# Kernel optimization log

Hardware: AMD Instinct MI355X
Metric: run time of the kernel (lower is better)

## Reference

```python
import jax, jax.numpy as jnp
import numpy as np

B, S, D, H = 32, 512, 256, 512  # batch, seq_len, input_dim, hidden_dim (512 hardcoded in source)


def setup_inputs() -> dict:
    key = jax.random.key(0)
    ks = jax.random.split(key, 24)
    sc = 1.0 / np.sqrt(H)

    def p(k, shape):
        return (jax.random.normal(k, shape, jnp.float32) * sc).astype(jnp.float32)

    return {
        "x": jax.random.normal(ks[0], (B, S, D), jnp.float32),
        # encoder forward direction (PyTorch LSTM gate order i,f,g,o)
        "Wih_f": p(ks[1], (4 * H, D)), "Whh_f": p(ks[2], (4 * H, H)), "b_f": p(ks[3], (4 * H,)),
        # encoder reverse direction
        "Wih_r": p(ks[4], (4 * H, D)), "Whh_r": p(ks[5], (4 * H, H)), "b_r": p(ks[6], (4 * H,)),
        # decoder LSTM (input never used: decoder_input is always zeros in the source)
        "Wih_d": p(ks[7], (4 * H, H)), "Whh_d": p(ks[8], (4 * H, H)), "b_d": p(ks[9], (4 * H,)),
        # reduce_h / reduce_c
        "Wr_h": p(ks[10], (H, 2 * H)), "br_h": p(ks[11], (H,)),
        "Wr_c": p(ks[12], (H, 2 * H)), "br_c": p(ks[13], (H,)),
        # pointer attention
        "W1": p(ks[14], (H, H)), "b1": p(ks[15], (H,)),
        "W2": p(ks[16], (H, H)), "b2": p(ks[17], (H,)),
        "vt": p(ks[18], (1, H)), "bvt": p(ks[19], (1,)),
    }


def _lstm_cell(h, c, z):
    i, f, g, o = jnp.split(z, 4, axis=-1)
    c_new = jax.nn.sigmoid(f) * c + jax.nn.sigmoid(i) * jnp.tanh(g)
    h_new = jax.nn.sigmoid(o) * jnp.tanh(c_new)
    return h_new, c_new


def _run_lstm(xs, Wih, Whh, b):
    """xs: [S, B, D] -> (outputs [S,B,H], h_T [B,H], c_T [B,H])"""
    Bn = xs.shape[1]
    Hn = Whh.shape[1]
    init = (jnp.zeros((Bn, Hn), xs.dtype), jnp.zeros((Bn, Hn), xs.dtype))
    x_proj = jnp.einsum('sbd,gd->sbg', xs, Wih) + b  # precompute input contribution

    def step(carry, xp):
        h, c = carry
        h, c = _lstm_cell(h, c, xp + h @ Whh.T)
        return (h, c), h

    (hT, cT), hs = jax.lax.scan(step, init, x_proj)
    return hs, hT, cT


def reference(x, Wih_f, Whh_f, b_f, Wih_r, Whh_r, b_r,
              Wih_d, Whh_d, b_d, Wr_h, br_h, Wr_c, br_c,
              W1, b1, W2, b2, vt, bvt):
    xs = jnp.swapaxes(x, 0, 1)  # [S, B, D]
    hs_f, hf, cf = _run_lstm(xs, Wih_f, Whh_f, b_f)
    hs_r, hr, cr = _run_lstm(xs[::-1], Wih_r, Whh_r, b_r)
    hs_r = hs_r[::-1]

    h_d = jnp.concatenate([hf, hr], axis=-1) @ Wr_h.T + br_h  # [B, H]
    c_d = jnp.concatenate([cf, cr], axis=-1) @ Wr_c.T + br_c

    enc_red = hs_f + hs_r  # [S, B, H]  (enc_out[...,:512] + enc_out[...,512:])
    pre1 = jnp.einsum('sbh,kh->sbk', enc_red, W1) + b1  # W1(enc) precomputed once

    seq_len = x.shape[1]

    def dec_step(carry, _):
        h, c = carry
        # decoder_input is always zeros -> Wih_d contribution is exactly 0
        h, c = _lstm_cell(h, c, h @ Whh_d.T + b_d)
        att = jnp.tanh(pre1 + (h @ W2.T + b2)[None])      # [S, B, H]
        scores = jnp.einsum('sbh,h->sb', att, vt[0]) + bvt[0]
        return (h, c), scores.T  # [B, S]

    _, logits = jax.lax.scan(dec_step, (h_d, c_d), None, length=seq_len)
    return jnp.swapaxes(logits, 0, 1)  # [B, seq_len, S]
```

## Files before the change

### kernel.cpp

```cpp
#include <hip/hip_runtime.h>
#include <hip/hip_bf16.h>
#include <cstdint>
#include <cstddef>

#define B_ 32
#define S_ 512
#define D_ 256
#define H_ 512

typedef _Float16 h2 __attribute__((ext_vector_type(2)));
typedef _Float16 h4 __attribute__((ext_vector_type(4)));
typedef _Float16 h8 __attribute__((ext_vector_type(8)));
typedef float f32x4 __attribute__((ext_vector_type(4)));
typedef unsigned u32x4 __attribute__((ext_vector_type(4)));

__device__ __forceinline__ h2 H2(unsigned u) { return __builtin_bit_cast(h2, u); }
__device__ __forceinline__ unsigned U2(h2 v) { return __builtin_bit_cast(unsigned, v); }

#if __has_builtin(__builtin_amdgcn_fdot2)
__device__ __forceinline__ float dot2f(h2 a, h2 b, float c) {
  return __builtin_amdgcn_fdot2(a, b, c, false);
}
#else
__device__ __forceinline__ float dot2f(h2 a, h2 b, float c) {
  return c + (float)a.x * (float)b.x + (float)a.y * (float)b.y;
}
#endif

#if __has_builtin(__builtin_amdgcn_exp2f)
__device__ __forceinline__ float exp2_fast(float x) { return __builtin_amdgcn_exp2f(x); }
#else
__device__ __forceinline__ float exp2_fast(float x) { return exp2f(x); }
#endif
#if __has_builtin(__builtin_amdgcn_rcpf)
__device__ __forceinline__ float rcp_fast(float x) { return __builtin_amdgcn_rcpf(x); }
#else
__device__ __forceinline__ float rcp_fast(float x) { return 1.0f / x; }
#endif

__device__ __forceinline__ float sigm(float x) {
  return rcp_fast(1.0f + exp2_fast(-1.4426950408889634f * x));
}
__device__ __forceinline__ float tanh_fast(float x) {
  return 1.0f - 2.0f * rcp_fast(1.0f + exp2_fast(2.8853900817779268f * x));
}

__device__ __forceinline__ uint4 coh_load16(const void* p) {
  u32x4 v;
  asm volatile("global_load_dwordx4 %0, %1, off sc0 sc1"
               : "=v"(v) : "v"(p) : "memory");
  return __builtin_bit_cast(uint4, v);
}
__device__ __forceinline__ void vm_drain() {
  asm volatile("s_waitcnt vmcnt(0)" ::: "memory");
}

__device__ __forceinline__ bool valid16(uint4 v) {
  return ((v.x & 0xFFFFu) != 0xFFFFu) && ((v.x >> 16) != 0xFFFFu) &&
         ((v.y & 0xFFFFu) != 0xFFFFu) && ((v.y >> 16) != 0xFFFFu) &&
         ((v.z & 0xFFFFu) != 0xFFFFu) && ((v.z >> 16) != 0xFFFFu) &&
         ((v.w & 0xFFFFu) != 0xFFFFu) && ((v.w >> 16) != 0xFFFFu);
}

__device__ __forceinline__ void h_store(unsigned short* p, unsigned short v) {
  __hip_atomic_store(p, v, __ATOMIC_RELAXED, __HIP_MEMORY_SCOPE_AGENT);
}

__global__ __launch_bounds__(256) void fill_sent_k(uint4* __restrict__ dst, size_t n16) {
  uint4 s = {0xFFFFFFFFu, 0xFFFFFFFFu, 0xFFFFFFFFu, 0xFFFFFFFFu};
  size_t stride = (size_t)gridDim.x * 256;
  for (size_t i = (size_t)blockIdx.x * 256 + threadIdx.x; i < n16; i += stride)
    dst[i] = s;
}

__global__ __launch_bounds__(256) void f2h_k(const float* __restrict__ src,
                                             _Float16* __restrict__ dst, int n4) {
  int i = blockIdx.x * 256 + threadIdx.x;
  if (i < n4) {
    float4 v = ((const float4*)src)[i];
    h4 o = {(_Float16)v.x, (_Float16)v.y, (_Float16)v.z, (_Float16)v.w};
    ((h4*)dst)[i] = o;
  }
}

__global__ __launch_bounds__(256, 1) void enc_coop_k(
    const _Float16* __restrict__ xh,
    const _Float16* __restrict__ WihF, const _Float16* __restrict__ WhhF, const float* __restrict__ bF,
    const _Float16* __restrict__ WihR, const _Float16* __restrict__ WhhR, const float* __restrict__ bR,
    float* __restrict__ cF, float* __restrict__ cR,
    _Float16* __restrict__ hsF, _Float16* __restrict__ hsR)
{
  __shared__ __align__(16) _Float16 cbuf[96][16][8];
  __shared__ float zfin[4][16][17];
  __shared__ float cls[16][17];

  const int bid = blockIdx.x;
  const int group = bid >> 5;
  const int dir = group >> 1;
  const int bh0 = (group & 1) << 4;
  const int jb = bid & 31;
  const int c0 = jb << 4;
  const int tid = threadIdx.x;
  const int lane = tid & 63;
  const int wv = tid >> 6;

  const _Float16* __restrict__ Wih = dir ? WihR : WihF;
  const _Float16* __restrict__ Whh = dir ? WhhR : WhhF;
  const float* __restrict__ bias = dir ? bR : bF;
  _Float16* __restrict__ hs = dir ? hsR : hsF;
  float* __restrict__ cOut = dir ? cR : cF;

  h8 aw[24];
  {
    const int m = lane & 15, kg = lane >> 4;
    const int wrow = wv * H_ + c0 + m;
    const _Float16* wi = Wih + (size_t)wrow * D_;
    const _Float16* wh = Whh + (size_t)wrow * H_;
    #pragma unroll
    for (int tu = 0; tu < 24; ++tu) {
      int k = tu * 32 + kg * 8;
      aw[tu] = (k < 256) ? *(const h8*)(wi + k) : *(const h8*)(wh + (k - 256));
    }
  }

  const int cc = tid & 15, cb = tid >> 4;
  float bvg[4];
  #pragma unroll
  for (int g = 0; g < 4; ++g) bvg[g] = bias[g * H_ + c0 + cc];

  const char* cbase = (const char*)cbuf + (size_t)((lane >> 4) * 256 + (lane & 15) * 16);
  const int sn = tid & 15;
  const int xo = (tid >> 4) * 2;
  const int ho = (tid >> 4) * 4;
  __syncthreads();

  for (int t = 0; t < S_; ++t) {
    const int xi = dir ? (S_ - 1 - t) : t;

    {
      const _Float16* xp = xh + ((size_t)(bh0 + sn) * S_ + xi) * D_;
      uint4 v0 = *(const uint4*)(xp + xo * 8);
      uint4 v1 = *(const uint4*)(xp + xo * 8 + 8);
      *(uint4*)&cbuf[xo][sn][0] = v0;
      *(uint4*)&cbuf[xo + 1][sn][0] = v1;
    }
    __syncthreads();

    f32x4 acc = {0.f, 0.f, 0.f, 0.f};
    #pragma unroll
    for (int tu = 0; tu < 8; ++tu) {
      h8 bf = *(const h8*)(cbase + tu * 1024);
      acc = __builtin_amdgcn_mfma_f32_16x16x32_f16(aw[tu], bf, acc, 0, 0, 0);
    }

    {
      if (t == 0) {
        uint4 z = {0, 0, 0, 0};
        #pragma unroll
        for (int u = 0; u < 4; ++u) *(uint4*)&cbuf[32 + ho + u][sn][0] = z;
      } else {
        const int xip = dir ? xi + 1 : xi - 1;
        const _Float16* hbase = hs + ((size_t)xip * B_ + bh0 + sn) * H_;
        uint4 vs[4];
        unsigned pend = 0xF;
        do {
          #pragma unroll
          for (int u = 0; u < 4; ++u)
            if (pend & (1u << u)) vs[u] = coh_load16(hbase + (ho + u) * 8);
          vm_drain();
          #pragma unroll
          for (int u = 0; u < 4; ++u)
            if ((pend & (1u << u)) && valid16(vs[u])) pend &= ~(1u << u);
        } while (pend);
        #pragma unroll
        for (int u = 0; u < 4; ++u) *(uint4*)&cbuf[32 + ho + u][sn][0] = vs[u];
      }
    }
    __syncthreads();

    #pragma unroll
    for (int tu = 8; tu < 24; ++tu) {
      h8 bf = *(const h8*)(cbase + tu * 1024);
      acc = __builtin_amdgcn_mfma_f32_16x16x32_f16(aw[tu], bf, acc, 0, 0, 0);
    }
    {
      const int mrow = (lane >> 4) * 4, n = lane & 15;
      #pragma unroll
      for (int r = 0; r < 4; ++r) zfin[wv][mrow + r][n] = acc[r];
    }
    __syncthreads();

    {
      const float zi = zfin[0][cc][cb] + bvg[0];
      const float zf = zfin[1][cc][cb] + bvg[1];
      const float zg = zfin[2][cc][cb] + bvg[2];
      const float zo = zfin[3][cc][cb] + bvg[3];
      const float c_old = (t == 0) ? 0.f : cls[cc][cb];
      const float cn = sigm(zf) * c_old + sigm(zi) * tanh_fast(zg);
      const float hn = sigm(zo) * tanh_fast(cn);
      cls[cc][cb] = cn;
      _Float16 hh = (_Float16)hn;
      h_store((unsigned short*)(hs + ((size_t)xi * B_ + bh0 + cb) * H_ + c0 + cc),
              __builtin_bit_cast(unsigned short, hh));
      if (t == S_ - 1) cOut[(size_t)(bh0 + cb) * H_ + c0 + cc] = cn;
    }
    __syncthreads();
  }
}

__global__ __launch_bounds__(256, 1) void dec_coop_k(
    const float* __restrict__ hd0, const float* __restrict__ cD0,
    const _Float16* __restrict__ Whh, const float* __restrict__ bias,
    _Float16* __restrict__ hdec)
{
  __shared__ __align__(16) _Float16 cbuf[64][16][8];
  __shared__ float zfin[4][16][17];
  __shared__ float cls[16][17];

  const int bid = blockIdx.x;
  const int group = bid >> 5;
  const int bh0 = group << 4;
  const int jb = bid & 31;
  const int c0 = jb << 4;
  const int tid = threadIdx.x;
  const int lane = tid & 63;
  const int wv = tid >> 6;

  h8 aw[16];
  {
    const int m = lane & 15, kg = lane >> 4;
    const _Float16* wh = Whh + (size_t)(wv * H_ + c0 + m) * H_;
    #pragma unroll
    for (int tu = 0; tu < 16; ++tu) aw[tu] = *(const h8*)(wh + tu * 32 + kg * 8);
  }

  const int cc = tid & 15, cb = tid >> 4;
  float bvg[4];
  #pragma unroll
  for (int g = 0; g < 4; ++g) bvg[g] = bias[g * H_ + c0 + cc];
  cls[cc][cb] = cD0[(size_t)(bh0 + cb) * H_ + c0 + cc];

  const char* cbase = (const char*)cbuf + (size_t)((lane >> 4) * 256 + (lane & 15) * 16);
  const int sn = tid & 15, ho = (tid >> 4) * 4;
  __syncthreads();

  for (int t = 0; t < S_; ++t) {
    {
      if (t == 0) {
        const float* src = hd0 + (size_t)(bh0 + sn) * H_;
        #pragma unroll
        for (int u = 0; u < 4; ++u) {
          float4 f0 = *(const float4*)(src + (ho + u) * 8);
          float4 f1 = *(const float4*)(src + (ho + u) * 8 + 4);
          h8 o = {(_Float16)f0.x, (_Float16)f0.y, (_Float16)f0.z, (_Float16)f0.w,
                  (_Float16)f1.x, (_Float16)f1.y, (_Float16)f1.z, (_Float16)f1.w};
          *(h8*)&cbuf[ho + u][sn][0] = o;
        }
      } else {
        const _Float16* src = hdec + ((size_t)(t - 1) * B_ + bh0 + sn) * H_;
        uint4 vs[4];
        unsigned pend = 0xF;
        do {
          #pragma unroll
          for (int u = 0; u < 4; ++u)
            if (pend & (1u << u)) vs[u] = coh_load16(src + (ho + u) * 8);
          vm_drain();
          #pragma unroll
          for (int u = 0; u < 4; ++u)
            if ((pend & (1u << u)) && valid16(vs[u])) pend &= ~(1u << u);
        } while (pend);
        #pragma unroll
        for (int u = 0; u < 4; ++u) *(uint4*)&cbuf[ho + u][sn][0] = vs[u];
      }
    }
    __syncthreads();

    f32x4 acc = {0.f, 0.f, 0.f, 0.f};
    #pragma unroll
    for (int tu = 0; tu < 16; ++tu) {
      h8 bf = *(const h8*)(cbase + tu * 1024);
      acc = __builtin_amdgcn_mfma_f32_16x16x32_f16(aw[tu], bf, acc, 0, 0, 0);
    }
    {
      const int mrow = (lane >> 4) * 4, n = lane & 15;
      #pragma unroll
      for (int r = 0; r < 4; ++r) zfin[wv][mrow + r][n] = acc[r];
    }
    __syncthreads();

    {
      const float zi = zfin[0][cc][cb] + bvg[0];
      const float zf = zfin[1][cc][cb] + bvg[1];
      const float zg = zfin[2][cc][cb] + bvg[2];
      const float zo = zfin[3][cc][cb] + bvg[3];
      const float cn = sigm(zf) * cls[cc][cb] + sigm(zi) * tanh_fast(zg);
      const float hn = sigm(zo) * tanh_fast(cn);
      cls[cc][cb] = cn;
      _Float16 hh = (_Float16)hn;
      h_store((unsigned short*)(hdec + ((size_t)t * B_ + bh0 + cb) * H_ + c0 + cc),
              __builtin_bit_cast(unsigned short, hh));
    }
    __syncthreads();
  }
}

template <int MODE>
__global__ __launch_bounds__(256) void gemm_h_k(
    const _Float16* __restrict__ A1, const _Float16* __restrict__ A2,
    const _Float16* __restrict__ W, const float* __restrict__ bias,
    _Float16* __restrict__ C)
{
  __shared__ h2 As2[16][68];
  __shared__ h2 Bs2[16][68];
  const int tid = threadIdx.x;
  const int m0 = blockIdx.x * 64, n0 = blockIdx.y * 64;
  const int tn = tid & 15, tm = tid >> 4;
  float acc[4][4] = {};

  for (int kc = 0; kc < H_; kc += 32) {
    __syncthreads();
    {
      int mm = tid >> 2, q = tid & 3;
      uint4 a = *(const uint4*)(A1 + (size_t)(m0 + mm) * H_ + kc + q * 8);
      if (MODE == 1) {
        uint4 a2 = *(const uint4*)(A2 + (size_t)(m0 + mm) * H_ + kc + q * 8);
        a.x = U2(H2(a.x) + H2(a2.x)); a.y = U2(H2(a.y) + H2(a2.y));
        a.z = U2(H2(a.z) + H2(a2.z)); a.w = U2(H2(a.w) + H2(a2.w));
      }
      As2[q * 4 + 0][mm] = H2(a.x); As2[q * 4 + 1][mm] = H2(a.y);
      As2[q * 4 + 2][mm] = H2(a.z); As2[q * 4 + 3][mm] = H2(a.w);
      uint4 b = *(const uint4*)(W + (size_t)(n0 + mm) * H_ + kc + q * 8);
      Bs2[q * 4 + 0][mm] = H2(b.x); Bs2[q * 4 + 1][mm] = H2(b.y);
      Bs2[q * 4 + 2][mm] = H2(b.z); Bs2[q * 4 + 3][mm] = H2(b.w);
    }
    __syncthreads();
    #pragma unroll
    for (int k2 = 0; k2 < 16; ++k2) {
      uint4 au = *(const uint4*)&As2[k2][tm * 4];
      uint4 bu = *(const uint4*)&Bs2[k2][tn * 4];
      h2 a[4] = {H2(au.x), H2(au.y), H2(au.z), H2(au.w)};
      h2 b[4] = {H2(bu.x), H2(bu.y), H2(bu.z), H2(bu.w)};
      #pragma unroll
      for (int i = 0; i < 4; ++i)
        #pragma unroll
        for (int j = 0; j < 4; ++j)
          acc[i][j] = dot2f(a[i], b[j], acc[i][j]);
    }
  }
  float4 bl = *(const float4*)(bias + n0 + tn * 4);
  #pragma unroll
  for (int i = 0; i < 4; ++i) {
    h2 p0 = {(_Float16)(acc[i][0] + bl.x), (_Float16)(acc[i][1] + bl.y)};
    h2 p1 = {(_Float16)(acc[i][2] + bl.z), (_Float16)(acc[i][3] + bl.w)};
    uint2 st = {U2(p0), U2(p1)};
    *(uint2*)(C + (size_t)(m0 + tm * 4 + i) * H_ + n0 + tn * 4) = st;
  }
}

__device__ __forceinline__ float4 load4f(const float* p) { return *(const float4*)p; }
__device__ __forceinline__ float4 load4f(const _Float16* p) {
  uint2 u = *(const uint2*)p;
  h2 a = H2(u.x), b = H2(u.y);
  return make_float4((float)a.x, (float)a.y, (float)b.x, (float)b.y);
}

template <typename T>
__global__ __launch_bounds__(256) void gemm_cat_small_k(
    const T* __restrict__ A1, const T* __restrict__ A2,
    const float* __restrict__ W, const float* __restrict__ bias,
    float* __restrict__ C)
{
  const int tid = threadIdx.x;
  const int col = tid & 31;
  const int rg  = tid >> 5;
  const int n   = blockIdx.y * 32 + col;
  float acc[4] = {0, 0, 0, 0};
  #pragma unroll
  for (int pass = 0; pass < 2; ++pass) {
    const T* __restrict__ A = pass ? A2 : A1;
    const float4* __restrict__ w4 = (const float4*)(W + (size_t)n * 1024 + pass * 512);
    for (int k4 = 0; k4 < 128; ++k4) {
      float4 w = w4[k4];
      #pragma unroll
      for (int i = 0; i < 4; ++i) {
        int row = rg + (i << 3);
        float4 a = load4f(A + (size_t)row * H_ + k4 * 4);
        acc[i] += w.x * a.x + w.y * a.y + w.z * a.z + w.w * a.w;
      }
    }
  }
  const float bv = bias[n];
  #pragma unroll
  for (int i = 0; i < 4; ++i) {
    int row = rg + (i << 3);
    C[(size_t)row * H_ + n] = acc[i] + bv;
  }
}

__global__ __launch_bounds__(256) void attn_k(
    const _Float16* __restrict__ pre1, const _Float16* __restrict__ Qm,
    const float* __restrict__ vt, const float* __restrict__ bvt,
    float* __restrict__ out)
{
  __shared__ float sp[16][260];
  __shared__ float sq[16][260];
  __shared__ float sv[256];
  const int b = blockIdx.z, tbase = blockIdx.y << 4, sbase = blockIdx.x << 4;
  const int tid = threadIdx.x;
  const int so = tid & 15;
  const int to = tid >> 4;
  float acc = 0.f;

  for (int h0 = 0; h0 < H_; h0 += 256) {
    __syncthreads();
    {
      int i = tid >> 4, off = (tid & 15) * 16;
      uint4 q0 = *(const uint4*)(Qm + ((size_t)(tbase + i) * B_ + b) * H_ + h0 + off);
      uint4 q1 = *(const uint4*)(Qm + ((size_t)(tbase + i) * B_ + b) * H_ + h0 + off + 8);
      uint4 p0 = *(const uint4*)(pre1 + ((size_t)(sbase + i) * B_ + b) * H_ + h0 + off);
      uint4 p1 = *(const uint4*)(pre1 + ((size_t)(sbase + i) * B_ + b) * H_ + h0 + off + 8);
      const unsigned* qs = (const unsigned*)&q0;
      const unsigned* ps = (const unsigned*)&p0;
      #pragma unroll
      for (int u = 0; u < 4; ++u) {
        h2 qv = H2(qs[u]), pv = H2(ps[u]);
        sq[i][off + u * 2] = (float)qv.x; sq[i][off + u * 2 + 1] = (float)qv.y;
        sp[i][off + u * 2] = (float)pv.x; sp[i][off + u * 2 + 1] = (float)pv.y;
      }
      const unsigned* qs2 = (const unsigned*)&q1;
      const unsigned* ps2 = (const unsigned*)&p1;
      #pragma unroll
      for (int u = 0; u < 4; ++u) {
        h2 qv = H2(qs2[u]), pv = H2(ps2[u]);
        sq[i][off + 8 + u * 2] = (float)qv.x; sq[i][off + 8 + u * 2 + 1] = (float)qv.y;
        sp[i][off + 8 + u * 2] = (float)pv.x; sp[i][off + 8 + u * 2 + 1] = (float)pv.y;
      }
    }
    sv[tid] = vt[h0 + tid];
    __syncthreads();
    #pragma unroll 4
    for (int h = 0; h < 256; ++h)
      acc += sv[h] * tanh_fast(sp[so][h] + sq[to][h]);
  }
  out[((size_t)b * S_ + tbase + to) * S_ + sbase + so] = acc + bvt[0];
}

extern "C" void kernel_launch(void* const* d_in, const int* in_sizes, int n_in,
                              void* d_out, int out_size, void* d_ws, size_t ws_size,
                              hipStream_t stream)
{
  (void)in_sizes; (void)n_in; (void)out_size; (void)ws_size;
  const float* x     = (const float*)d_in[0];
  const float* WihF  = (const float*)d_in[1];
  const float* WhhF  = (const float*)d_in[2];
  const float* bF    = (const float*)d_in[3];
  const float* WihR  = (const float*)d_in[4];
  const float* WhhR  = (const float*)d_in[5];
  const float* bR    = (const float*)d_in[6];
  const float* WhhD  = (const float*)d_in[8];
  const float* bD    = (const float*)d_in[9];
  const float* Wr_h  = (const float*)d_in[10];
  const float* br_h  = (const float*)d_in[11];
  const float* Wr_c  = (const float*)d_in[12];
  const float* br_c  = (const float*)d_in[13];
  const float* W1    = (const float*)d_in[14];
  const float* b1    = (const float*)d_in[15];
  const float* W2    = (const float*)d_in[16];
  const float* b2    = (const float*)d_in[17];
  const float* vt    = (const float*)d_in[18];
  const float* bvt   = (const float*)d_in[19];
  float* out = (float*)d_out;

  const size_t SBH = (size_t)S_ * B_ * H_;
  const size_t BH  = (size_t)B_ * H_;

  _Float16* hp = (_Float16*)d_ws;
  _Float16* hs_f  = hp;              hp += SBH;
  _Float16* hs_r  = hp;              hp += SBH;
  _Float16* hdec  = hp;              hp += SBH;
  _Float16* pre1h = hp;              hp += SBH;
  _Float16* Qmh   = hp;              hp += SBH;
  _Float16* xh    = hp;              hp += (size_t)B_ * S_ * D_;
  _Float16* wihF  = hp;              hp += (size_t)4 * H_ * D_;
  _Float16* wihR  = hp;              hp += (size_t)4 * H_ * D_;
  _Float16* whhF  = hp;              hp += (size_t)4 * H_ * H_;
  _Float16* whhR  = hp;              hp += (size_t)4 * H_ * H_;
  _Float16* whhD  = hp;              hp += (size_t)4 * H_ * H_;
  _Float16* w1h   = hp;              hp += (size_t)H_ * H_;
  _Float16* w2h   = hp;              hp += (size_t)H_ * H_;
  float* fp  = (float*)hp;
  float* cF  = fp;                   fp += BH;
  float* cR  = fp;                   fp += BH;
  float* cD  = fp;                   fp += BH;
  float* hd0 = fp;                   fp += BH;

  fill_sent_k<<<2048, 256, 0, stream>>>((uint4*)hs_f, 3 * SBH / 8);

  f2h_k<<<(B_ * S_ * D_ / 4 + 255) / 256, 256, 0, stream>>>(x, xh, B_ * S_ * D_ / 4);
  f2h_k<<<(4 * H_ * D_ / 4 + 255) / 256, 256, 0, stream>>>(WihF, wihF, 4 * H_ * D_ / 4);
  f2h_k<<<(4 * H_ * D_ / 4 + 255) / 256, 256, 0, stream>>>(WihR, wihR, 4 * H_ * D_ / 4);
  f2h_k<<<(4 * H_ * H_ / 4 + 255) / 256, 256, 0, stream>>>(WhhF, whhF, 4 * H_ * H_ / 4);
  f2h_k<<<(4 * H_ * H_ / 4 + 255) / 256, 256, 0, stream>>>(WhhR, whhR, 4 * H_ * H_ / 4);
  f2h_k<<<(4 * H_ * H_ / 4 + 255) / 256, 256, 0, stream>>>(WhhD, whhD, 4 * H_ * H_ / 4);
  f2h_k<<<(H_ * H_ / 4 + 255) / 256, 256, 0, stream>>>(W1, w1h, H_ * H_ / 4);
  f2h_k<<<(H_ * H_ / 4 + 255) / 256, 256, 0, stream>>>(W2, w2h, H_ * H_ / 4);

  enc_coop_k<<<128, 256, 0, stream>>>(xh, wihF, whhF, bF, wihR, whhR, bR,
                                      cF, cR, hs_f, hs_r);

  gemm_cat_small_k<_Float16><<<dim3(1, 16), 256, 0, stream>>>(
      hs_f + (size_t)(S_ - 1) * BH, hs_r, Wr_h, br_h, hd0);
  gemm_cat_small_k<float><<<dim3(1, 16), 256, 0, stream>>>(cF, cR, Wr_c, br_c, cD);

  gemm_h_k<1><<<dim3(256, 8), 256, 0, stream>>>(hs_f, hs_r, w1h, b1, pre1h);

  dec_coop_k<<<64, 256, 0, stream>>>(hd0, cD, whhD, bD, hdec);

  gemm_h_k<0><<<dim3(256, 8), 256, 0, stream>>>(hdec, nullptr, w2h, b2, Qmh);

  attn_k<<<dim3(32, 32, 32), 256, 0, stream>>>(pre1h, Qmh, vt, bvt, out);
}
```

Baseline: 3.956 ms.

## Use MFMA for hidden GEMMs and factor attention tanh into exp products

Replaces the dot2-based 64x64 GEMM for the W1 and W2 projections with MFMA 16x16x32 f16 instructions that read K-major shared tiles. Rewrites the attention score so that tanh(p+q) becomes 1 - 2/(1 + e^{2p}·e^{2q}). The exponentials are precomputed per element when tiles are loaded, which leaves one fma and one rcp per inner iteration. The sum of vt is folded into a constant computed by a new tiny kernel. The exponent is clamped to ±60, which risks precision differences at large magnitudes.

```diff
diff --git a/kernel.cpp b/kernel.cpp
--- a/kernel.cpp
+++ b/kernel.cpp
@@ -16,16 +16,6 @@
 
 __device__ __forceinline__ h2 H2(unsigned u) { return __builtin_bit_cast(h2, u); }
 __device__ __forceinline__ unsigned U2(h2 v) { return __builtin_bit_cast(unsigned, v); }
-
-#if __has_builtin(__builtin_amdgcn_fdot2)
-__device__ __forceinline__ float dot2f(h2 a, h2 b, float c) {
-  return __builtin_amdgcn_fdot2(a, b, c, false);
-}
-#else
-__device__ __forceinline__ float dot2f(h2 a, h2 b, float c) {
-  return c + (float)a.x * (float)b.x + (float)a.y * (float)b.y;
-}
-#endif
 
 #if __has_builtin(__builtin_amdgcn_exp2f)
 __device__ __forceinline__ float exp2_fast(float x) { return __builtin_amdgcn_exp2f(x); }
@@ -305,55 +295,52 @@
 }
 
 template <int MODE>
-__global__ __launch_bounds__(256) void gemm_h_k(
+__global__ __launch_bounds__(256) void gemm_mfma_k(
     const _Float16* __restrict__ A1, const _Float16* __restrict__ A2,
     const _Float16* __restrict__ W, const float* __restrict__ bias,
     _Float16* __restrict__ C)
 {
-  __shared__ h2 As2[16][68];
-  __shared__ h2 Bs2[16][68];
+  __shared__ __align__(16) _Float16 Abuf[4][66][8];
+  __shared__ __align__(16) _Float16 Bbuf[4][66][8];
   const int tid = threadIdx.x;
   const int m0 = blockIdx.x * 64, n0 = blockIdx.y * 64;
-  const int tn = tid & 15, tm = tid >> 4;
-  float acc[4][4] = {};
+  const int lane = tid & 63, wv = tid >> 6;
+  const int sr = tid >> 2, sk = tid & 3;
+  f32x4 acc[4] = {{0.f,0.f,0.f,0.f},{0.f,0.f,0.f,0.f},
+                  {0.f,0.f,0.f,0.f},{0.f,0.f,0.f,0.f}};
 
   for (int kc = 0; kc < H_; kc += 32) {
     __syncthreads();
     {
-      int mm = tid >> 2, q = tid & 3;
-      uint4 a = *(const uint4*)(A1 + (size_t)(m0 + mm) * H_ + kc + q * 8);
+      uint4 a = *(const uint4*)(A1 + (size_t)(m0 + sr) * H_ + kc + sk * 8);
       if (MODE == 1) {
-        uint4 a2 = *(const uint4*)(A2 + (size_t)(m0 + mm) * H_ + kc + q * 8);
+        uint4 a2 = *(const uint4*)(A2 + (size_t)(m0 + sr) * H_ + kc + sk * 8);
         a.x = U2(H2(a.x) + H2(a2.x)); a.y = U2(H2(a.y) + H2(a2.y));
         a.z = U2(H2(a.z) + H2(a2.z)); a.w = U2(H2(a.w) + H2(a2.w));
       }
-      As2[q * 4 + 0][mm] = H2(a.x); As2[q * 4 + 1][mm] = H2(a.y);
-      As2[q * 4 + 2][mm] = H2(a.z); As2[q * 4 + 3][mm] = H2(a.w);
-      uint4 b = *(const uint4*)(W + (size_t)(n0 + mm) * H_ + kc + q * 8);
-      Bs2[q * 4 + 0][mm] = H2(b.x); Bs2[q * 4 + 1][mm] = H2(b.y);
-      Bs2[q * 4 + 2][mm] = H2(b.z); Bs2[q * 4 + 3][mm] = H2(b.w);
-    }
-    __syncthreads();
-    #pragma unroll
-    for (int k2 = 0; k2 < 16; ++k2) {
-      uint4 au = *(const uint4*)&As2[k2][tm * 4];
-      uint4 bu = *(const uint4*)&Bs2[k2][tn * 4];
-      h2 a[4] = {H2(au.x), H2(au.y), H2(au.z), H2(au.w)};
-      h2 b[4] = {H2(bu.x), H2(bu.y), H2(bu.z), H2(bu.w)};
-      #pragma unroll
-      for (int i = 0; i < 4; ++i)
-        #pragma unroll
-        for (int j = 0; j < 4; ++j)
-          acc[i][j] = dot2f(a[i], b[j], acc[i][j]);
-    }
-  }
-  float4 bl = *(const float4*)(bias + n0 + tn * 4);
+      *(uint4*)&Abuf[sk][sr][0] = a;
+      uint4 b = *(const uint4*)(W + (size_t)(n0 + sr) * H_ + kc + sk * 8);
+      *(uint4*)&Bbuf[sk][sr][0] = b;
+    }
+    __syncthreads();
+    const int fr = lane & 15, kg = lane >> 4;
+    h8 af = *(const h8*)&Abuf[kg][wv * 16 + fr][0];
+    #pragma unroll
+    for (int nt = 0; nt < 4; ++nt) {
+      h8 bf = *(const h8*)&Bbuf[kg][nt * 16 + fr][0];
+      acc[nt] = __builtin_amdgcn_mfma_f32_16x16x32_f16(af, bf, acc[nt], 0, 0, 0);
+    }
+  }
+  const int fr = lane & 15, fq = lane >> 4;
   #pragma unroll
-  for (int i = 0; i < 4; ++i) {
-    h2 p0 = {(_Float16)(acc[i][0] + bl.x), (_Float16)(acc[i][1] + bl.y)};
-    h2 p1 = {(_Float16)(acc[i][2] + bl.z), (_Float16)(acc[i][3] + bl.w)};
-    uint2 st = {U2(p0), U2(p1)};
-    *(uint2*)(C + (size_t)(m0 + tm * 4 + i) * H_ + n0 + tn * 4) = st;
+  for (int nt = 0; nt < 4; ++nt) {
+    const int n = n0 + nt * 16 + fr;
+    const float bv = bias[n];
+    #pragma unroll
+    for (int r = 0; r < 4; ++r) {
+      const int m = m0 + wv * 16 + fq * 4 + r;
+      C[(size_t)m * H_ + n] = (_Float16)(acc[nt][r] + bv);
+    }
   }
 }
 
@@ -397,52 +384,55 @@
   }
 }
 
+__global__ __launch_bounds__(256) void sumv_k(const float* __restrict__ vt,
+                                              float* __restrict__ o) {
+  __shared__ float sh[4];
+  float v = vt[threadIdx.x] + vt[threadIdx.x + 256];
+  #pragma unroll
+  for (int d = 32; d; d >>= 1) v += __shfl_down(v, d, 64);
+  if ((threadIdx.x & 63) == 0) sh[threadIdx.x >> 6] = v;
+  __syncthreads();
+  if (threadIdx.x == 0) o[0] = sh[0] + sh[1] + sh[2] + sh[3];
+}
+
+#define KT_ 2.8853900817779268f
 __global__ __launch_bounds__(256) void attn_k(
     const _Float16* __restrict__ pre1, const _Float16* __restrict__ Qm,
     const float* __restrict__ vt, const float* __restrict__ bvt,
-    float* __restrict__ out)
+    const float* __restrict__ sumv, float* __restrict__ out)
 {
   __shared__ float sp[16][260];
   __shared__ float sq[16][260];
   __shared__ float sv[256];
   const int b = blockIdx.z, tbase = blockIdx.y << 4, sbase = blockIdx.x << 4;
   const int tid = threadIdx.x;
-  const int so = tid & 15;
-  const int to = tid >> 4;
+  const int so = tid & 15, to = tid >> 4;
   float acc = 0.f;
+  const float cfin = sumv[0] + bvt[0];
 
   for (int h0 = 0; h0 < H_; h0 += 256) {
     __syncthreads();
     {
       int i = tid >> 4, off = (tid & 15) * 16;
-      uint4 q0 = *(const uint4*)(Qm + ((size_t)(tbase + i) * B_ + b) * H_ + h0 + off);
-      uint4 q1 = *(const uint4*)(Qm + ((size_t)(tbase + i) * B_ + b) * H_ + h0 + off + 8);
-      uint4 p0 = *(const uint4*)(pre1 + ((size_t)(sbase + i) * B_ + b) * H_ + h0 + off);
-      uint4 p1 = *(const uint4*)(pre1 + ((size_t)(sbase + i) * B_ + b) * H_ + h0 + off + 8);
-      const unsigned* qs = (const unsigned*)&q0;
-      const unsigned* ps = (const unsigned*)&p0;
+      const _Float16* qp = Qm + ((size_t)(tbase + i) * B_ + b) * H_ + h0 + off;
+      const _Float16* pp = pre1 + ((size_t)(sbase + i) * B_ + b) * H_ + h0 + off;
+      h8 q0 = *(const h8*)qp, q1 = *(const h8*)(qp + 8);
+      h8 p0 = *(const h8*)pp, p1 = *(const h8*)(pp + 8);
       #pragma unroll
-      for (int u = 0; u < 4; ++u) {
-        h2 qv = H2(qs[u]), pv = H2(ps[u]);
-        sq[i][off + u * 2] = (float)qv.x; sq[i][off + u * 2 + 1] = (float)qv.y;
-        sp[i][off + u * 2] = (float)pv.x; sp[i][off + u * 2 + 1] = (float)pv.y;
-      }
-      const unsigned* qs2 = (const unsigned*)&q1;
-      const unsigned* ps2 = (const unsigned*)&p1;
-      #pragma unroll
-      for (int u = 0; u < 4; ++u) {
-        h2 qv = H2(qs2[u]), pv = H2(ps2[u]);
-        sq[i][off + 8 + u * 2] = (float)qv.x; sq[i][off + 8 + u * 2 + 1] = (float)qv.y;
-        sp[i][off + 8 + u * 2] = (float)pv.x; sp[i][off + 8 + u * 2 + 1] = (float)pv.y;
+      for (int j = 0; j < 8; ++j) {
+        sq[i][off + j]     = exp2_fast(fminf(fmaxf(KT_ * (float)q0[j], -60.f), 60.f));
+        sq[i][off + 8 + j] = exp2_fast(fminf(fmaxf(KT_ * (float)q1[j], -60.f), 60.f));
+        sp[i][off + j]     = exp2_fast(fminf(fmaxf(KT_ * (float)p0[j], -60.f), 60.f));
+        sp[i][off + 8 + j] = exp2_fast(fminf(fmaxf(KT_ * (float)p1[j], -60.f), 60.f));
       }
     }
     sv[tid] = vt[h0 + tid];
     __syncthreads();
     #pragma unroll 4
     for (int h = 0; h < 256; ++h)
-      acc += sv[h] * tanh_fast(sp[so][h] + sq[to][h]);
-  }
-  out[((size_t)b * S_ + tbase + to) * S_ + sbase + so] = acc + bvt[0];
+      acc = fmaf(sv[h], rcp_fast(fmaf(sp[so][h], sq[to][h], 1.0f)), acc);
+  }
+  out[((size_t)b * S_ + tbase + to) * S_ + sbase + so] = cfin - 2.f * acc;
 }
 
 extern "C" void kernel_launch(void* const* d_in, const int* in_sizes, int n_in,
@@ -493,6 +483,7 @@
   float* cR  = fp;                   fp += BH;
   float* cD  = fp;                   fp += BH;
   float* hd0 = fp;                   fp += BH;
+  float* sumv = fp;
 
   fill_sent_k<<<2048, 256, 0, stream>>>((uint4*)hs_f, 3 * SBH / 8);
 
@@ -504,6 +495,7 @@
   f2h_k<<<(4 * H_ * H_ / 4 + 255) / 256, 256, 0, stream>>>(WhhD, whhD, 4 * H_ * H_ / 4);
   f2h_k<<<(H_ * H_ / 4 + 255) / 256, 256, 0, stream>>>(W1, w1h, H_ * H_ / 4);
   f2h_k<<<(H_ * H_ / 4 + 255) / 256, 256, 0, stream>>>(W2, w2h, H_ * H_ / 4);
+  sumv_k<<<1, 256, 0, stream>>>(vt, sumv);
 
   enc_coop_k<<<128, 256, 0, stream>>>(xh, wihF, whhF, bF, wihR, whhR, bR,
                                       cF, cR, hs_f, hs_r);
@@ -512,11 +504,11 @@
       hs_f + (size_t)(S_ - 1) * BH, hs_r, Wr_h, br_h, hd0);
   gemm_cat_small_k<float><<<dim3(1, 16), 256, 0, stream>>>(cF, cR, Wr_c, br_c, cD);
 
-  gemm_h_k<1><<<dim3(256, 8), 256, 0, stream>>>(hs_f, hs_r, w1h, b1, pre1h);
+  gemm_mfma_k<1><<<dim3(256, 8), 256, 0, stream>>>(hs_f, hs_r, w1h, b1, pre1h);
 
   dec_coop_k<<<64, 256, 0, stream>>>(hd0, cD, whhD, bD, hdec);
 
-  gemm_h_k<0><<<dim3(256, 8), 256, 0, stream>>>(hdec, nullptr, w2h, b2, Qmh);
-
-  attn_k<<<dim3(32, 32, 32), 256, 0, stream>>>(pre1h, Qmh, vt, bvt, out);
-}
+  gemm_mfma_k<0><<<dim3(256, 8), 256, 0, stream>>>(hdec, nullptr, w2h, b2, Qmh);
+
+  attn_k<<<dim3(32, 32, 32), 256, 0, stream>>>(pre1h, Qmh, vt, bvt, sumv, out);
+}
```

New measurement: 3.480 ms. 12.0% less time.
